# Kernel tuning notes

Measured on AMD Instinct MI355X. Metric: run time of the kernel, lower is better.

Reference implementation:

```python
import jax, jax.numpy as jnp
import numpy as np

NEG_SLOPE = 0.1

def lrelu(x):
    return jnp.where(x >= 0, x, NEG_SLOPE * x)

def conv1d(x, w, b, stride=2):
    # x: [N, C_in, W], w: [C_out, C_in, K], VALID padding, given stride
    y = jax.lax.conv_general_dilated(x, w, (stride,), 'VALID',
                                     dimension_numbers=('NCH', 'OIH', 'NCH'))
    return y + b[None, :, None]

def setup_inputs() -> dict:
    key = jax.random.key(0)
    ks = jax.random.split(key, 16)
    N_NODES = 50000
    N_EDGES = 4950000
    POS_C, CONV_C, CONV_W = 3, 3, 151
    HID, OUT = 256, 1
    W2 = 37  # width after two stride-2 k=3 convs on 151
    IN_G = POS_C + W2  # 40

    def lin_init(k, fan_out, fan_in):
        s = 1.0 / np.sqrt(fan_in)
        k1, k2 = jax.random.split(k)
        return (jax.random.uniform(k1, (fan_out, fan_in), jnp.float32, -s, s),
                jax.random.uniform(k2, (fan_out,), jnp.float32, -s, s))

    pose = jax.random.normal(ks[0], (N_NODES, POS_C), jnp.float32)
    views = jax.random.normal(ks[1], (N_NODES, CONV_C, CONV_W), jnp.float32)
    edge_index = jax.random.randint(ks[2], (2, N_EDGES), 0, N_NODES, jnp.int64)

    # encoder1: Conv1d(3 -> 9, k=3, s=2); encoder2: Conv1d(9 -> 1, k=3, s=2)
    s1 = 1.0 / np.sqrt(CONV_C * 3)
    w_e1 = jax.random.uniform(ks[3], (CONV_C ** 2, CONV_C, 3), jnp.float32, -s1, s1)
    b_e1 = jax.random.uniform(ks[4], (CONV_C ** 2,), jnp.float32, -s1, s1)
    s2 = 1.0 / np.sqrt(CONV_C ** 2 * 3)
    w_e2 = jax.random.uniform(ks[5], (1, CONV_C ** 2, 3), jnp.float32, -s2, s2)
    b_e2 = jax.random.uniform(ks[6], (1,), jnp.float32, -s2, s2)

    # GraphConv: lin_rel (with bias) on aggregated neighbors, lin_root (no bias) on self
    w_rel, b_rel = lin_init(ks[7], HID, IN_G)
    w_root, _ = lin_init(ks[8], HID, IN_G)

    w_l1, b_l1 = lin_init(ks[9], HID, HID)
    w_l2, b_l2 = lin_init(ks[10], HID, HID)
    w_l3, b_l3 = lin_init(ks[11], HID, HID)
    w_pred, b_pred = lin_init(ks[12], OUT, HID)

    return dict(pose=pose, views=views, edge_index=edge_index,
                w_e1=w_e1, b_e1=b_e1, w_e2=w_e2, b_e2=b_e2,
                w_rel=w_rel, b_rel=b_rel, w_root=w_root,
                w_l1=w_l1, b_l1=b_l1, w_l2=w_l2, b_l2=b_l2,
                w_l3=w_l3, b_l3=b_l3, w_pred=w_pred, b_pred=b_pred)

def reference(pose, views, edge_index, w_e1, b_e1, w_e2, b_e2,
              w_rel, b_rel, w_root,
              w_l1, b_l1, w_l2, b_l2, w_l3, b_l3, w_pred, b_pred):
    n_nodes = pose.shape[0]
    # view encoder
    v = lrelu(conv1d(views, w_e1, b_e1))          # [N, 9, 75]
    v = lrelu(conv1d(v, w_e2, b_e2))              # [N, 1, 37]
    x = jnp.concatenate([pose, v[:, 0, :]], axis=1)  # [N, 40]
    # GraphConv (aggr='add'): out = lin_rel(sum_{j->i} x_j) + lin_root(x_i)
    src, dst = edge_index[0], edge_index[1]
    agg = jax.ops.segment_sum(x[src], dst, num_segments=n_nodes)  # [N, 40]
    h = lrelu(agg @ w_rel.T + b_rel + x @ w_root.T)               # [N, 256]
    # MLP stack (dropout is identity in eval mode)
    h = lrelu(h @ w_l1.T + b_l1)
    h = lrelu(h @ w_l2.T + b_l2)
    h = lrelu(h @ w_l3.T + b_l3)
    return h @ w_pred.T + b_pred  # [N, 1]
```

## Files before the change

### kernel.cpp

```cpp
#include <hip/hip_runtime.h>
#include <hip/hip_fp16.h>

#define NEG_SLOPE 0.1f
__device__ __forceinline__ float lrelu(float v) { return fmaxf(v, NEG_SLOPE * v); }

constexpr int CAP = 8704;
constexpr int EPB = 8192;

typedef __attribute__((ext_vector_type(8))) short short8;
typedef __attribute__((ext_vector_type(4))) float f32x4;

__device__ __forceinline__ unsigned short f2bf(float f) {
    union { float f; unsigned u; } v; v.f = f;
    const unsigned r = v.u + 0x7FFF + ((v.u >> 16) & 1);
    return (unsigned short)(r >> 16);
}
__device__ __forceinline__ float bf2f(unsigned short h) {
    union { unsigned u; float f; } v; v.u = ((unsigned)h) << 16;
    return v.f;
}

struct BinSmem {
    int hist[1024], loff[1024], base[1024];
    int wave8[8];
    int pk[EPB];
    unsigned short bkt[EPB];
};
struct EncSmem {
    float w1[81], b1v[9], w2[27], b2v[1];
    float c1[8][9][80];
};

__global__ __launch_bounds__(512) void enc_bin_kernel(
        const int* __restrict__ ei, int* __restrict__ gcur,
        int* __restrict__ pairs, int E, int NB, int NBIN,
        const float* __restrict__ pose, const float* __restrict__ views,
        const float* __restrict__ w1, const float* __restrict__ b1,
        const float* __restrict__ w2, const float* __restrict__ b2,
        const float* __restrict__ w_l1, const float* __restrict__ w_l2,
        const float* __restrict__ w_l3, const float* __restrict__ w_rel,
        const float* __restrict__ w_root,
        unsigned short* __restrict__ Wb1, unsigned short* __restrict__ Wb2,
        unsigned short* __restrict__ Wb3, unsigned short* __restrict__ Wg,
        unsigned short* __restrict__ xHi, unsigned short* __restrict__ xLo,
        __half* __restrict__ xh, int N)
{
    __shared__ __align__(16) char smem_raw[sizeof(BinSmem)];
    const int t = threadIdx.x;

    if (blockIdx.x < (unsigned)NBIN) {
        BinSmem& sm = *reinterpret_cast<BinSmem*>(smem_raw);
        const int lane = t & 63, wid = t >> 6;
        const int e0 = blockIdx.x * EPB + t * 16;
        const int tot = min(E - (int)blockIdx.x * EPB, EPB);

        for (int i = t; i < 1024; i += 512) sm.hist[i] = 0;
        __syncthreads();

        int pk[16], mt[16];
        auto proc = [&](int j, int sv, int dv) {
            const int b = dv >> 6;
            const int r = atomicAdd(&sm.hist[b], 1);
            pk[j] = sv * 80 | ((dv & 63) << 22);
            mt[j] = b | (r << 10);
        };

        if (e0 + 16 <= E) {
            #pragma unroll
            for (int q = 0; q < 4; q++) {
                const int4 sv = *(const int4*)(ei + e0 + 4 * q);
                const int4 dv = *(const int4*)(ei + E + e0 + 4 * q);
                proc(4 * q + 0, sv.x, dv.x);
                proc(4 * q + 1, sv.y, dv.y);
                proc(4 * q + 2, sv.z, dv.z);
                proc(4 * q + 3, sv.w, dv.w);
            }
        } else {
            #pragma unroll
            for (int j = 0; j < 16; j++) {
                mt[j] = -1;
                const int e = e0 + j;
                if (e < E) proc(j, ei[e], ei[E + e]);
            }
        }
        __syncthreads();

        int carry = 0;
        #pragma unroll
        for (int base = 0; base < 1024; base += 512) {
            const int i = base + t;
            const int v = sm.hist[i];
            int sc = v;
            #pragma unroll
            for (int d = 1; d < 64; d <<= 1) {
                const int u = __shfl_up(sc, d);
                if (lane >= d) sc += u;
            }
            if (lane == 63) sm.wave8[wid] = sc;
            __syncthreads();
            if (wid == 0) {
                int wv = (lane < 8) ? sm.wave8[lane] : 0;
                #pragma unroll
                for (int d = 1; d < 8; d <<= 1) {
                    const int u = __shfl_up(wv, d);
                    if (lane >= d) wv += u;
                }
                if (lane < 8) sm.wave8[lane] = wv;
            }
            __syncthreads();
            const int waveoff = (wid > 0) ? sm.wave8[wid - 1] : 0;
            sm.loff[i] = carry + waveoff + sc - v;
            const int chunk_tot = sm.wave8[7];
            __syncthreads();
            carry += chunk_tot;
        }

        for (int i = t; i < NB; i += 512) {
            const int c = sm.hist[i];
            if (c > 0) sm.base[i] = atomicAdd(&gcur[i], c);
        }
        __syncthreads();

        #pragma unroll
        for (int j = 0; j < 16; j++) {
            if (mt[j] >= 0) {
                const int b = mt[j] & 1023;
                const int pos = sm.loff[b] + (mt[j] >> 10);
                sm.pk[pos] = pk[j];
                sm.bkt[pos] = (unsigned short)b;
            }
        }
        __syncthreads();

        for (int i = t; i < tot; i += 512) {
            const int b = sm.bkt[i];
            const int p = sm.base[b] + (i - sm.loff[b]);
            if (p < CAP) pairs[b * CAP + p] = sm.pk[i];
        }
        return;
    }

    EncSmem& sm = *reinterpret_cast<EncSmem*>(smem_raw);
    const int eb = blockIdx.x - NBIN;

    if (eb < 128) {
        const int i = eb * 512 + t;
        Wb1[i] = f2bf(w_l1[i]);
        Wb2[i] = f2bf(w_l2[i]);
        Wb3[i] = f2bf(w_l3[i]);
        if (i < 40960) {
            const int m = i / 160, c = i % 160;
            const int k = c % 80;
            const float v = (k < 40) ? w_rel[m * 40 + k] : w_root[m * 40 + (k - 40)];
            Wg[i] = f2bf(v);
        }
        if (eb == 0 && t < 40) xh[(size_t)N * 40 + t] = __float2half(0.f);
    }

    if (t < 81) sm.w1[t] = w1[t];
    if (t >= 96 && t < 105) sm.b1v[t - 96] = b1[t - 96];
    if (t >= 128 && t < 155) sm.w2[t - 128] = w2[t - 128];
    if (t == 240) sm.b2v[0] = b2[0];
    __syncthreads();

    const int nb = eb * 8;

    #pragma unroll
    for (int pass = 0; pass < 2; pass++) {
        const int task = pass * 512 + t;
        if (task < 600) {
            const int ln = task / 75;
            const int p  = task % 75;
            const int n  = min(nb + ln, N - 1);
            const float* __restrict__ vin = views + (size_t)n * 453 + 2 * p;
            float e[3], o[3], e1[3];
            #pragma unroll
            for (int ic = 0; ic < 3; ic++) {
                const float* ci = vin + ic * 151;
                e[ic] = ci[0]; o[ic] = ci[1]; e1[ic] = ci[2];
            }
            const int didx = (p & 1) * 40 + (p >> 1);
            #pragma unroll
            for (int oc = 0; oc < 9; oc++) {
                float v = sm.b1v[oc];
                #pragma unroll
                for (int ic = 0; ic < 3; ic++)
                    v += sm.w1[oc * 9 + ic * 3 + 0] * e[ic]
                       + sm.w1[oc * 9 + ic * 3 + 1] * o[ic]
                       + sm.w1[oc * 9 + ic * 3 + 2] * e1[ic];
                sm.c1[ln][oc][didx] = lrelu(v);
            }
        }
    }
    __syncthreads();

    if (t < 320) {
        const int ln = t / 40, f = t % 40;
        const int n  = min(nb + ln, N - 1);
        float outv;
        if (f < 3) {
            outv = pose[(size_t)n * 3 + f];
        } else {
            const int ow = f - 3;
            float v = sm.b2v[0];
            #pragma unroll
            for (int ic = 0; ic < 9; ic++)
                v += sm.w2[ic * 3 + 0] * sm.c1[ln][ic][ow]
                   + sm.w2[ic * 3 + 1] * sm.c1[ln][ic][40 + ow]
                   + sm.w2[ic * 3 + 2] * sm.c1[ln][ic][ow + 1];
            outv = lrelu(v);
        }
        const unsigned short hi = f2bf(outv);
        const unsigned short lo = f2bf(outv - bf2f(hi));
        xHi[(size_t)n * 40 + f] = hi;
        xLo[(size_t)n * 40 + f] = lo;
        xh[(size_t)n * 40 + f] = __float2half(outv);
    }
}

__global__ void bucket_sort_kernel(const int* __restrict__ gcur,
                                   const int* __restrict__ pairs,
                                   int* __restrict__ sorted,
                                   int* __restrict__ node_start,
                                   int* __restrict__ node_cnt, int N)
{
    __shared__ int s_cnt[64], s_off[64], s_cur[64];
    const int b = blockIdx.x;
    const int t = threadIdx.x;
    const int cnt = min(gcur[b], CAP);
    const int* __restrict__ pr = pairs + b * CAP;
    int* __restrict__ so = sorted + (size_t)b * CAP;

    if (t < 64) s_cnt[t] = 0;
    __syncthreads();
    for (int i = t; i < cnt; i += 256)
        atomicAdd(&s_cnt[pr[i] >> 22], 1);
    __syncthreads();

    if (t < 64) {
        const int c = s_cnt[t];
        const int p = ((c + 23) / 24) * 24;
        int sc = p;
        #pragma unroll
        for (int d = 1; d < 64; d <<= 1) {
            const int u = __shfl_up(sc, d);
            if (t >= d) sc += u;
        }
        const int excl = sc - p;
        s_off[t] = excl;
        s_cur[t] = excl;
        node_start[b * 64 + t] = b * CAP + excl;
        node_cnt[b * 64 + t] = c;
    }
    __syncthreads();

    if (t < 64) {
        const int e0 = s_off[t] + s_cnt[t];
        const int e1 = s_off[t] + ((s_cnt[t] + 23) / 24) * 24;
        for (int i = e0; i < e1 && i < CAP; i++) so[i] = N * 80;
    }
    for (int i = t; i < cnt; i += 256) {
        const int p = pr[i];
        const int pos = atomicAdd(&s_cur[p >> 22], 1);
        if (pos < CAP) so[pos] = p & 0x3FFFFF;
    }
}

__global__ void gather_sum_kernel(const int* __restrict__ sorted,
                                  const int* __restrict__ node_start,
                                  const int* __restrict__ node_cnt,
                                  const __half* __restrict__ xh,
                                  unsigned short* __restrict__ aggHi,
                                  unsigned short* __restrict__ aggLo, int N)
{
    const int n = blockIdx.x * 4 + (threadIdx.x >> 6);
    const int lane = threadIdx.x & 63;
    if (n >= N) return;

    const int start = node_start[n];
    const int cntp = ((node_cnt[n] + 23) / 24) * 24;
    const int slot = min(lane / 10, 5);
    const int f4 = lane % 10;
    const int* __restrict__ srt = sorted + start + slot;
    const char* __restrict__ xb = (const char*)xh + f4 * 8;

    float ax = 0.f, ay = 0.f, az = 0.f, aw = 0.f;
    for (int e = 0; e < cntp; e += 24) {
        const int o0 = srt[e];
        const int o1 = srt[e + 6];
        const int o2 = srt[e + 12];
        const int o3 = srt[e + 18];
        const uint2 u0 = *(const uint2*)(xb + o0);
        const uint2 u1 = *(const uint2*)(xb + o1);
        const uint2 u2 = *(const uint2*)(xb + o2);
        const uint2 u3 = *(const uint2*)(xb + o3);
        union { unsigned u; __half2 h; } c;
        float2 f;
        c.u = u0.x; f = __half22float2(c.h); ax += f.x; ay += f.y;
        c.u = u0.y; f = __half22float2(c.h); az += f.x; aw += f.y;
        c.u = u1.x; f = __half22float2(c.h); ax += f.x; ay += f.y;
        c.u = u1.y; f = __half22float2(c.h); az += f.x; aw += f.y;
        c.u = u2.x; f = __half22float2(c.h); ax += f.x; ay += f.y;
        c.u = u2.y; f = __half22float2(c.h); az += f.x; aw += f.y;
        c.u = u3.x; f = __half22float2(c.h); ax += f.x; ay += f.y;
        c.u = u3.y; f = __half22float2(c.h); az += f.x; aw += f.y;
    }

    float rx = ax, ry = ay, rz = az, rw = aw;
    #pragma unroll
    for (int s = 10; s <= 50; s += 10) {
        rx += __shfl(ax, f4 + s);
        ry += __shfl(ay, f4 + s);
        rz += __shfl(az, f4 + s);
        rw += __shfl(aw, f4 + s);
    }
    if (lane < 10) {
        ushort4 hi, lo;
        hi.x = f2bf(rx); lo.x = f2bf(rx - bf2f(hi.x));
        hi.y = f2bf(ry); lo.y = f2bf(ry - bf2f(hi.y));
        hi.z = f2bf(rz); lo.z = f2bf(rz - bf2f(hi.z));
        hi.w = f2bf(rw); lo.w = f2bf(rw - bf2f(hi.w));
        *(ushort4*)(aggHi + (size_t)n * 40 + f4 * 4) = hi;
        *(ushort4*)(aggLo + (size_t)n * 40 + f4 * 4) = lo;
    }
}

__device__ __forceinline__ void gemm_tile(const unsigned short* __restrict__ aT,
                                          const unsigned short* __restrict__ W,
                                          int wstride, int K,
                                          int wave, int l16, int q,
                                          f32x4 acc[4][4])
{
    for (int k0 = 0; k0 < K; k0 += 32) {
        short8 af[4], wf[4];
        #pragma unroll
        for (int nt = 0; nt < 4; nt++)
            af[nt] = *(const short8*)(aT + (nt * 16 + l16) * 264 + k0 + q * 8);
        #pragma unroll
        for (int mt = 0; mt < 4; mt++)
            wf[mt] = *(const short8*)(W + (wave * 64 + mt * 16 + l16) * wstride + k0 + q * 8);
        #pragma unroll
        for (int nt = 0; nt < 4; nt++)
            #pragma unroll
            for (int mt = 0; mt < 4; mt++)
                acc[nt][mt] = __builtin_amdgcn_mfma_f32_16x16x32_bf16(af[nt], wf[mt], acc[nt][mt], 0, 0, 0);
    }
}

__device__ __forceinline__ void epi_to_lds(f32x4 acc[4][4], const float* __restrict__ b,
                                           unsigned short* __restrict__ aT,
                                           int wave, int l16, int q)
{
    float bias[4];
    #pragma unroll
    for (int mt = 0; mt < 4; mt++) bias[mt] = b[wave * 64 + mt * 16 + l16];
    #pragma unroll
    for (int nt = 0; nt < 4; nt++)
        #pragma unroll
        for (int r = 0; r < 4; r++)
            #pragma unroll
            for (int mt = 0; mt < 4; mt++) {
                const int row = nt * 16 + q * 4 + r;
                const int col = wave * 64 + mt * 16 + l16;
                aT[row * 264 + col] = f2bf(lrelu(acc[nt][mt][r] + bias[mt]));
            }
}

__global__ void fused_gemm_kernel(const unsigned short* __restrict__ aggHi,
                                  const unsigned short* __restrict__ aggLo,
                                  const unsigned short* __restrict__ xHi,
                                  const unsigned short* __restrict__ xLo,
                                  const unsigned short* __restrict__ Wg,
                                  const float* __restrict__ b_rel,
                                  const unsigned short* __restrict__ Wb1,
                                  const float* __restrict__ b_l1,
                                  const unsigned short* __restrict__ Wb2,
                                  const float* __restrict__ b_l2,
                                  const unsigned short* __restrict__ Wb3,
                                  const float* __restrict__ b_l3,
                                  const float* __restrict__ w_pred,
                                  const float* __restrict__ b_pred,
                                  float* __restrict__ out, int N)
{
    __shared__ __align__(16) unsigned short aT[64 * 264];
    __shared__ float s_part[4][64];
    const int t = threadIdx.x;
    const int n0 = blockIdx.x * 64;
    const int wave = t >> 6, lane = t & 63, q = lane >> 4, l16 = lane & 15;

    for (int u = t; u < 640; u += 256) {
        const int row = u / 10, c = (u % 10) * 4;
        const int srow = min(n0 + row, N - 1);
        const size_t off = (size_t)srow * 40 + c;
        unsigned short* rp = aT + row * 264;
        *(ushort4*)(rp + c)       = *(const ushort4*)(aggHi + off);
        *(ushort4*)(rp + 40 + c)  = *(const ushort4*)(xHi + off);
        *(ushort4*)(rp + 80 + c)  = *(const ushort4*)(aggLo + off);
        *(ushort4*)(rp + 120 + c) = *(const ushort4*)(xLo + off);
    }
    __syncthreads();

    {
        f32x4 acc[4][4] = {};
        gemm_tile(aT, Wg, 160, 160, wave, l16, q, acc);
        __syncthreads();
        epi_to_lds(acc, b_rel, aT, wave, l16, q);
        __syncthreads();
    }
    {
        f32x4 acc[4][4] = {};
        gemm_tile(aT, Wb1, 256, 256, wave, l16, q, acc);
        __syncthreads();
        epi_to_lds(acc, b_l1, aT, wave, l16, q);
        __syncthreads();
    }
    {
        f32x4 acc[4][4] = {};
        gemm_tile(aT, Wb2, 256, 256, wave, l16, q, acc);
        __syncthreads();
        epi_to_lds(acc, b_l2, aT, wave, l16, q);
        __syncthreads();
    }
    {
        f32x4 acc[4][4] = {};
        gemm_tile(aT, Wb3, 256, 256, wave, l16, q, acc);

        float bias[4], wp[4];
        #pragma unroll
        for (int mt = 0; mt < 4; mt++) {
            const int col = wave * 64 + mt * 16 + l16;
            bias[mt] = b_l3[col];
            wp[mt] = w_pred[col];
        }
        #pragma unroll
        for (int nt = 0; nt < 4; nt++)
            #pragma unroll
            for (int r = 0; r < 4; r++) {
                float p = 0.f;
                #pragma unroll
                for (int mt = 0; mt < 4; mt++)
                    p += lrelu(acc[nt][mt][r] + bias[mt]) * wp[mt];
                p += __shfl_xor(p, 1);
                p += __shfl_xor(p, 2);
                p += __shfl_xor(p, 4);
                p += __shfl_xor(p, 8);
                if (l16 == 0) s_part[wave][nt * 16 + q * 4 + r] = p;
            }
        __syncthreads();

        if (t < 64) {
            const int row = n0 + t;
            if (row < N)
                out[row] = s_part[0][t] + s_part[1][t] + s_part[2][t] + s_part[3][t] + b_pred[0];
        }
    }
}

extern "C" void kernel_launch(void* const* d_in, const int* in_sizes, int n_in,
                              void* d_out, int out_size, void* d_ws, size_t ws_size,
                              hipStream_t stream)
{
    const float* pose   = (const float*)d_in[0];
    const float* views  = (const float*)d_in[1];
    const int*   ei     = (const int*)d_in[2];
    const float* w_e1   = (const float*)d_in[3];
    const float* b_e1   = (const float*)d_in[4];
    const float* w_e2   = (const float*)d_in[5];
    const float* b_e2   = (const float*)d_in[6];
    const float* w_rel  = (const float*)d_in[7];
    const float* b_rel  = (const float*)d_in[8];
    const float* w_root = (const float*)d_in[9];
    const float* w_l1   = (const float*)d_in[10];
    const float* b_l1   = (const float*)d_in[11];
    const float* w_l2   = (const float*)d_in[12];
    const float* b_l2   = (const float*)d_in[13];
    const float* w_l3   = (const float*)d_in[14];
    const float* b_l3   = (const float*)d_in[15];
    const float* w_pred = (const float*)d_in[16];
    const float* b_pred = (const float*)d_in[17];
    float* out = (float*)d_out;

    const int N = in_sizes[0] / 3;
    const int E = in_sizes[2] / 2;
    const int NB = (N + 63) >> 6;
    const int NBIN = (E + EPB - 1) / EPB;
    const int ENCB = (N + 7) / 8;
    const int NBLK = (N + 63) / 64;

    unsigned short* xHi = (unsigned short*)d_ws;
    unsigned short* xLo = xHi + (size_t)N * 40;
    unsigned short* aggHi = xLo + (size_t)N * 40;
    unsigned short* aggLo = aggHi + (size_t)N * 40;
    __half* xh = (__half*)(aggLo + (size_t)N * 40);
    int* pairs  = (int*)(xh + (size_t)(N + 1) * 40 + 24);
    int* sorted = pairs + (size_t)NB * CAP;
    int* gcur       = sorted + (size_t)NB * CAP;
    int* node_start = gcur + 1024;
    int* node_cnt   = node_start + NB * 64;
    unsigned short* Wb1 = (unsigned short*)(node_cnt + NB * 64);
    unsigned short* Wb2 = Wb1 + 256 * 256;
    unsigned short* Wb3 = Wb2 + 256 * 256;
    unsigned short* Wg  = Wb3 + 256 * 256;

    hipMemsetAsync(gcur, 0, 1024 * sizeof(int), stream);

    enc_bin_kernel<<<NBIN + ENCB, 512, 0, stream>>>(
        ei, gcur, pairs, E, NB, NBIN,
        pose, views, w_e1, b_e1, w_e2, b_e2,
        w_l1, w_l2, w_l3, w_rel, w_root,
        Wb1, Wb2, Wb3, Wg,
        xHi, xLo, xh, N);

    bucket_sort_kernel<<<NB, 256, 0, stream>>>(gcur, pairs, sorted, node_start, node_cnt, N);
    gather_sum_kernel<<<NB * 16, 256, 0, stream>>>(sorted, node_start, node_cnt, xh, aggHi, aggLo, N);

    fused_gemm_kernel<<<NBLK, 256, 0, stream>>>(
        aggHi, aggLo, xHi, xLo, Wg, b_rel,
        Wb1, b_l1, Wb2, b_l2, Wb3, b_l3,
        w_pred, b_pred, out, N);
}
```

Measured before the change: 370.4 us.

## Fuse bucket sort with gather-sum in shared memory and split encoder from binning

```diff
diff --git a/kernel.cpp b/kernel.cpp
--- a/kernel.cpp
+++ b/kernel.cpp
@@ -20,21 +20,9 @@
     return v.f;
 }
 
-struct BinSmem {
-    int hist[1024], loff[1024], base[1024];
-    int wave8[8];
-    int pk[EPB];
-    unsigned short bkt[EPB];
-};
-struct EncSmem {
-    float w1[81], b1v[9], w2[27], b2v[1];
-    float c1[8][9][80];
-};
-
-__global__ __launch_bounds__(512) void enc_bin_kernel(
-        const int* __restrict__ ei, int* __restrict__ gcur,
-        int* __restrict__ pairs, int E, int NB, int NBIN,
-        const float* __restrict__ pose, const float* __restrict__ views,
+__global__ __launch_bounds__(256) void encoder_kernel(
+        const float* __restrict__ pose,
+        const float* __restrict__ views,
         const float* __restrict__ w1, const float* __restrict__ b1,
         const float* __restrict__ w2, const float* __restrict__ b2,
         const float* __restrict__ w_l1, const float* __restrict__ w_l2,
@@ -42,109 +30,20 @@
         const float* __restrict__ w_root,
         unsigned short* __restrict__ Wb1, unsigned short* __restrict__ Wb2,
         unsigned short* __restrict__ Wb3, unsigned short* __restrict__ Wg,
+        int* __restrict__ gcur,
         unsigned short* __restrict__ xHi, unsigned short* __restrict__ xLo,
         __half* __restrict__ xh, int N)
 {
-    __shared__ __align__(16) char smem_raw[sizeof(BinSmem)];
+    __shared__ float s_w1[81];
+    __shared__ float s_b1[9];
+    __shared__ float s_w2[27];
+    __shared__ float s_b2[1];
+    __shared__ float s_c1[4][9][80];
+
     const int t = threadIdx.x;
 
-    if (blockIdx.x < (unsigned)NBIN) {
-        BinSmem& sm = *reinterpret_cast<BinSmem*>(smem_raw);
-        const int lane = t & 63, wid = t >> 6;
-        const int e0 = blockIdx.x * EPB + t * 16;
-        const int tot = min(E - (int)blockIdx.x * EPB, EPB);
-
-        for (int i = t; i < 1024; i += 512) sm.hist[i] = 0;
-        __syncthreads();
-
-        int pk[16], mt[16];
-        auto proc = [&](int j, int sv, int dv) {
-            const int b = dv >> 6;
-            const int r = atomicAdd(&sm.hist[b], 1);
-            pk[j] = sv * 80 | ((dv & 63) << 22);
-            mt[j] = b | (r << 10);
-        };
-
-        if (e0 + 16 <= E) {
-            #pragma unroll
-            for (int q = 0; q < 4; q++) {
-                const int4 sv = *(const int4*)(ei + e0 + 4 * q);
-                const int4 dv = *(const int4*)(ei + E + e0 + 4 * q);
-                proc(4 * q + 0, sv.x, dv.x);
-                proc(4 * q + 1, sv.y, dv.y);
-                proc(4 * q + 2, sv.z, dv.z);
-                proc(4 * q + 3, sv.w, dv.w);
-            }
-        } else {
-            #pragma unroll
-            for (int j = 0; j < 16; j++) {
-                mt[j] = -1;
-                const int e = e0 + j;
-                if (e < E) proc(j, ei[e], ei[E + e]);
-            }
-        }
-        __syncthreads();
-
-        int carry = 0;
-        #pragma unroll
-        for (int base = 0; base < 1024; base += 512) {
-            const int i = base + t;
-            const int v = sm.hist[i];
-            int sc = v;
-            #pragma unroll
-            for (int d = 1; d < 64; d <<= 1) {
-                const int u = __shfl_up(sc, d);
-                if (lane >= d) sc += u;
-            }
-            if (lane == 63) sm.wave8[wid] = sc;
-            __syncthreads();
-            if (wid == 0) {
-                int wv = (lane < 8) ? sm.wave8[lane] : 0;
-                #pragma unroll
-                for (int d = 1; d < 8; d <<= 1) {
-                    const int u = __shfl_up(wv, d);
-                    if (lane >= d) wv += u;
-                }
-                if (lane < 8) sm.wave8[lane] = wv;
-            }
-            __syncthreads();
-            const int waveoff = (wid > 0) ? sm.wave8[wid - 1] : 0;
-            sm.loff[i] = carry + waveoff + sc - v;
-            const int chunk_tot = sm.wave8[7];
-            __syncthreads();
-            carry += chunk_tot;
-        }
-
-        for (int i = t; i < NB; i += 512) {
-            const int c = sm.hist[i];
-            if (c > 0) sm.base[i] = atomicAdd(&gcur[i], c);
-        }
-        __syncthreads();
-
-        #pragma unroll
-        for (int j = 0; j < 16; j++) {
-            if (mt[j] >= 0) {
-                const int b = mt[j] & 1023;
-                const int pos = sm.loff[b] + (mt[j] >> 10);
-                sm.pk[pos] = pk[j];
-                sm.bkt[pos] = (unsigned short)b;
-            }
-        }
-        __syncthreads();
-
-        for (int i = t; i < tot; i += 512) {
-            const int b = sm.bkt[i];
-            const int p = sm.base[b] + (i - sm.loff[b]);
-            if (p < CAP) pairs[b * CAP + p] = sm.pk[i];
-        }
-        return;
-    }
-
-    EncSmem& sm = *reinterpret_cast<EncSmem*>(smem_raw);
-    const int eb = blockIdx.x - NBIN;
-
-    if (eb < 128) {
-        const int i = eb * 512 + t;
+    if (blockIdx.x < 256) {
+        const int i = blockIdx.x * 256 + t;
         Wb1[i] = f2bf(w_l1[i]);
         Wb2[i] = f2bf(w_l2[i]);
         Wb3[i] = f2bf(w_l3[i]);
@@ -154,21 +53,22 @@
             const float v = (k < 40) ? w_rel[m * 40 + k] : w_root[m * 40 + (k - 40)];
             Wg[i] = f2bf(v);
         }
-        if (eb == 0 && t < 40) xh[(size_t)N * 40 + t] = __float2half(0.f);
-    }
-
-    if (t < 81) sm.w1[t] = w1[t];
-    if (t >= 96 && t < 105) sm.b1v[t - 96] = b1[t - 96];
-    if (t >= 128 && t < 155) sm.w2[t - 128] = w2[t - 128];
-    if (t == 240) sm.b2v[0] = b2[0];
-    __syncthreads();
-
-    const int nb = eb * 8;
+        if (i < 1024) gcur[i] = 0;
+        if (i < 40) xh[(size_t)N * 40 + i] = __float2half(0.f);
+    }
+
+    if (t < 81) s_w1[t] = w1[t];
+    if (t >= 96 && t < 105) s_b1[t - 96] = b1[t - 96];
+    if (t >= 128 && t < 155) s_w2[t - 128] = w2[t - 128];
+    if (t == 240) s_b2[0] = b2[0];
+    __syncthreads();
+
+    const int nb = blockIdx.x * 4;
 
     #pragma unroll
     for (int pass = 0; pass < 2; pass++) {
-        const int task = pass * 512 + t;
-        if (task < 600) {
+        const int task = pass * 256 + t;
+        if (task < 300) {
             const int ln = task / 75;
             const int p  = task % 75;
             const int n  = min(nb + ln, N - 1);
@@ -182,19 +82,19 @@
             const int didx = (p & 1) * 40 + (p >> 1);
             #pragma unroll
             for (int oc = 0; oc < 9; oc++) {
-                float v = sm.b1v[oc];
+                float v = s_b1[oc];
                 #pragma unroll
                 for (int ic = 0; ic < 3; ic++)
-                    v += sm.w1[oc * 9 + ic * 3 + 0] * e[ic]
-                       + sm.w1[oc * 9 + ic * 3 + 1] * o[ic]
-                       + sm.w1[oc * 9 + ic * 3 + 2] * e1[ic];
-                sm.c1[ln][oc][didx] = lrelu(v);
+                    v += s_w1[oc * 9 + ic * 3 + 0] * e[ic]
+                       + s_w1[oc * 9 + ic * 3 + 1] * o[ic]
+                       + s_w1[oc * 9 + ic * 3 + 2] * e1[ic];
+                s_c1[ln][oc][didx] = lrelu(v);
             }
         }
     }
     __syncthreads();
 
-    if (t < 320) {
+    if (t < 160) {
         const int ln = t / 40, f = t % 40;
         const int n  = min(nb + ln, N - 1);
         float outv;
@@ -202,12 +102,12 @@
             outv = pose[(size_t)n * 3 + f];
         } else {
             const int ow = f - 3;
-            float v = sm.b2v[0];
+            float v = s_b2[0];
             #pragma unroll
             for (int ic = 0; ic < 9; ic++)
-                v += sm.w2[ic * 3 + 0] * sm.c1[ln][ic][ow]
-                   + sm.w2[ic * 3 + 1] * sm.c1[ln][ic][40 + ow]
-                   + sm.w2[ic * 3 + 2] * sm.c1[ln][ic][ow + 1];
+                v += s_w2[ic * 3 + 0] * s_c1[ln][ic][ow]
+                   + s_w2[ic * 3 + 1] * s_c1[ln][ic][40 + ow]
+                   + s_w2[ic * 3 + 2] * s_c1[ln][ic][ow + 1];
             outv = lrelu(v);
         }
         const unsigned short hi = f2bf(outv);
@@ -218,22 +118,123 @@
     }
 }
 
-__global__ void bucket_sort_kernel(const int* __restrict__ gcur,
-                                   const int* __restrict__ pairs,
-                                   int* __restrict__ sorted,
-                                   int* __restrict__ node_start,
-                                   int* __restrict__ node_cnt, int N)
-{
+__global__ __launch_bounds__(512) void bin_kernel(
+        const int* __restrict__ ei, int* __restrict__ gcur,
+        int* __restrict__ pairs, int E, int NB)
+{
+    __shared__ int s_hist[1024];
+    __shared__ int s_loff[1024];
+    __shared__ int s_base[1024];
+    __shared__ int s_wave8[8];
+    __shared__ int s_pk[EPB];
+    __shared__ unsigned short s_bkt[EPB];
+    const int t = threadIdx.x;
+    const int lane = t & 63, wid = t >> 6;
+    const int e0 = blockIdx.x * EPB + t * 16;
+    const int tot = min(E - (int)blockIdx.x * EPB, EPB);
+
+    for (int i = t; i < 1024; i += 512) s_hist[i] = 0;
+    __syncthreads();
+
+    int pk[16], mt[16];
+    auto proc = [&](int j, int sv, int dv) {
+        const int b = dv >> 6;
+        const int r = atomicAdd(&s_hist[b], 1);
+        pk[j] = sv * 80 | ((dv & 63) << 22);
+        mt[j] = b | (r << 10);
+    };
+
+    if (e0 + 16 <= E) {
+        #pragma unroll
+        for (int q = 0; q < 4; q++) {
+            const int4 sv = *(const int4*)(ei + e0 + 4 * q);
+            const int4 dv = *(const int4*)(ei + E + e0 + 4 * q);
+            proc(4 * q + 0, sv.x, dv.x);
+            proc(4 * q + 1, sv.y, dv.y);
+            proc(4 * q + 2, sv.z, dv.z);
+            proc(4 * q + 3, sv.w, dv.w);
+        }
+    } else {
+        #pragma unroll
+        for (int j = 0; j < 16; j++) {
+            mt[j] = -1;
+            const int e = e0 + j;
+            if (e < E) proc(j, ei[e], ei[E + e]);
+        }
+    }
+    __syncthreads();
+
+    int carry = 0;
+    #pragma unroll
+    for (int base = 0; base < 1024; base += 512) {
+        const int i = base + t;
+        const int v = s_hist[i];
+        int sc = v;
+        #pragma unroll
+        for (int d = 1; d < 64; d <<= 1) {
+            const int u = __shfl_up(sc, d);
+            if (lane >= d) sc += u;
+        }
+        if (lane == 63) s_wave8[wid] = sc;
+        __syncthreads();
+        if (wid == 0) {
+            int wv = (lane < 8) ? s_wave8[lane] : 0;
+            #pragma unroll
+            for (int d = 1; d < 8; d <<= 1) {
+                const int u = __shfl_up(wv, d);
+                if (lane >= d) wv += u;
+            }
+            if (lane < 8) s_wave8[lane] = wv;
+        }
+        __syncthreads();
+        const int waveoff = (wid > 0) ? s_wave8[wid - 1] : 0;
+        s_loff[i] = carry + waveoff + sc - v;
+        const int chunk_tot = s_wave8[7];
+        __syncthreads();
+        carry += chunk_tot;
+    }
+
+    for (int i = t; i < NB; i += 512) {
+        const int c = s_hist[i];
+        if (c > 0) s_base[i] = atomicAdd(&gcur[i], c);
+    }
+    __syncthreads();
+
+    #pragma unroll
+    for (int j = 0; j < 16; j++) {
+        if (mt[j] >= 0) {
+            const int b = mt[j] & 1023;
+            const int pos = s_loff[b] + (mt[j] >> 10);
+            s_pk[pos] = pk[j];
+            s_bkt[pos] = (unsigned short)b;
+        }
+    }
+    __syncthreads();
+
+    for (int i = t; i < tot; i += 512) {
+        const int b = s_bkt[i];
+        const int p = s_base[b] + (i - s_loff[b]);
+        if (p < CAP) pairs[b * CAP + p] = s_pk[i];
+    }
+}
+
+__global__ __launch_bounds__(512) void sort_gather_kernel(
+        const int* __restrict__ gcur,
+        const int* __restrict__ pairs,
+        const __half* __restrict__ xh,
+        unsigned short* __restrict__ aggHi,
+        unsigned short* __restrict__ aggLo, int N)
+{
+    __shared__ int s_sorted[CAP];
     __shared__ int s_cnt[64], s_off[64], s_cur[64];
     const int b = blockIdx.x;
     const int t = threadIdx.x;
     const int cnt = min(gcur[b], CAP);
-    const int* __restrict__ pr = pairs + b * CAP;
-    int* __restrict__ so = sorted + (size_t)b * CAP;
+    const int* __restrict__ pr = pairs + (size_t)b * CAP;
 
     if (t < 64) s_cnt[t] = 0;
     __syncthreads();
-    for (int i = t; i < cnt; i += 256)
+    for (int i = t; i < cnt; i += 512)
         atomicAdd(&s_cnt[pr[i] >> 22], 1);
     __syncthreads();
 
@@ -249,79 +250,74 @@
         const int excl = sc - p;
         s_off[t] = excl;
         s_cur[t] = excl;
-        node_start[b * 64 + t] = b * CAP + excl;
-        node_cnt[b * 64 + t] = c;
     }
     __syncthreads();
 
     if (t < 64) {
         const int e0 = s_off[t] + s_cnt[t];
         const int e1 = s_off[t] + ((s_cnt[t] + 23) / 24) * 24;
-        for (int i = e0; i < e1 && i < CAP; i++) so[i] = N * 80;
-    }
-    for (int i = t; i < cnt; i += 256) {
+        for (int i = e0; i < e1 && i < CAP; i++) s_sorted[i] = N * 80;
+    }
+    for (int i = t; i < cnt; i += 512) {
         const int p = pr[i];
         const int pos = atomicAdd(&s_cur[p >> 22], 1);
-        if (pos < CAP) so[pos] = p & 0x3FFFFF;
-    }
-}
-
-__global__ void gather_sum_kernel(const int* __restrict__ sorted,
-                                  const int* __restrict__ node_start,
-                                  const int* __restrict__ node_cnt,
-                                  const __half* __restrict__ xh,
-                                  unsigned short* __restrict__ aggHi,
-                                  unsigned short* __restrict__ aggLo, int N)
-{
-    const int n = blockIdx.x * 4 + (threadIdx.x >> 6);
-    const int lane = threadIdx.x & 63;
-    if (n >= N) return;
-
-    const int start = node_start[n];
-    const int cntp = ((node_cnt[n] + 23) / 24) * 24;
+        if (pos < CAP) s_sorted[pos] = p & 0x3FFFFF;
+    }
+    __syncthreads();
+
+    const int wave = t >> 6, lane = t & 63;
     const int slot = min(lane / 10, 5);
     const int f4 = lane % 10;
-    const int* __restrict__ srt = sorted + start + slot;
     const char* __restrict__ xb = (const char*)xh + f4 * 8;
 
-    float ax = 0.f, ay = 0.f, az = 0.f, aw = 0.f;
-    for (int e = 0; e < cntp; e += 24) {
-        const int o0 = srt[e];
-        const int o1 = srt[e + 6];
-        const int o2 = srt[e + 12];
-        const int o3 = srt[e + 18];
-        const uint2 u0 = *(const uint2*)(xb + o0);
-        const uint2 u1 = *(const uint2*)(xb + o1);
-        const uint2 u2 = *(const uint2*)(xb + o2);
-        const uint2 u3 = *(const uint2*)(xb + o3);
-        union { unsigned u; __half2 h; } c;
-        float2 f;
-        c.u = u0.x; f = __half22float2(c.h); ax += f.x; ay += f.y;
-        c.u = u0.y; f = __half22float2(c.h); az += f.x; aw += f.y;
-        c.u = u1.x; f = __half22float2(c.h); ax += f.x; ay += f.y;
-        c.u = u1.y; f = __half22float2(c.h); az += f.x; aw += f.y;
-        c.u = u2.x; f = __half22float2(c.h); ax += f.x; ay += f.y;
-        c.u = u2.y; f = __half22float2(c.h); az += f.x; aw += f.y;
-        c.u = u3.x; f = __half22float2(c.h); ax += f.x; ay += f.y;
-        c.u = u3.y; f = __half22float2(c.h); az += f.x; aw += f.y;
-    }
-
-    float rx = ax, ry = ay, rz = az, rw = aw;
-    #pragma unroll
-    for (int s = 10; s <= 50; s += 10) {
-        rx += __shfl(ax, f4 + s);
-        ry += __shfl(ay, f4 + s);
-        rz += __shfl(az, f4 + s);
-        rw += __shfl(aw, f4 + s);
-    }
-    if (lane < 10) {
-        ushort4 hi, lo;
-        hi.x = f2bf(rx); lo.x = f2bf(rx - bf2f(hi.x));
-        hi.y = f2bf(ry); lo.y = f2bf(ry - bf2f(hi.y));
-        hi.z = f2bf(rz); lo.z = f2bf(rz - bf2f(hi.z));
-        hi.w = f2bf(rw); lo.w = f2bf(rw - bf2f(hi.w));
-        *(ushort4*)(aggHi + (size_t)n * 40 + f4 * 4) = hi;
-        *(ushort4*)(aggLo + (size_t)n * 40 + f4 * 4) = lo;
+    #pragma unroll 1
+    for (int i = 0; i < 8; i++) {
+        const int ln = wave * 8 + i;
+        const int n = b * 64 + ln;
+        if (n >= N) break;
+        const int c = s_cnt[ln];
+        const int cntp = ((c + 23) / 24) * 24;
+        const int* __restrict__ srt = s_sorted + s_off[ln] + slot;
+
+        float ax = 0.f, ay = 0.f, az = 0.f, aw = 0.f;
+        for (int e = 0; e < cntp; e += 24) {
+            const int o0 = srt[e];
+            const int o1 = srt[e + 6];
+            const int o2 = srt[e + 12];
+            const int o3 = srt[e + 18];
+            const uint2 u0 = *(const uint2*)(xb + o0);
+            const uint2 u1 = *(const uint2*)(xb + o1);
+            const uint2 u2 = *(const uint2*)(xb + o2);
+            const uint2 u3 = *(const uint2*)(xb + o3);
+            union { unsigned u; __half2 h; } cv;
+            float2 f;
+            cv.u = u0.x; f = __half22float2(cv.h); ax += f.x; ay += f.y;
+            cv.u = u0.y; f = __half22float2(cv.h); az += f.x; aw += f.y;
+            cv.u = u1.x; f = __half22float2(cv.h); ax += f.x; ay += f.y;
+            cv.u = u1.y; f = __half22float2(cv.h); az += f.x; aw += f.y;
+            cv.u = u2.x; f = __half22float2(cv.h); ax += f.x; ay += f.y;
+            cv.u = u2.y; f = __half22float2(cv.h); az += f.x; aw += f.y;
+            cv.u = u3.x; f = __half22float2(cv.h); ax += f.x; ay += f.y;
+            cv.u = u3.y; f = __half22float2(cv.h); az += f.x; aw += f.y;
+        }
+
+        float rx = ax, ry = ay, rz = az, rw = aw;
+        #pragma unroll
+        for (int s = 10; s <= 50; s += 10) {
+            rx += __shfl(ax, f4 + s);
+            ry += __shfl(ay, f4 + s);
+            rz += __shfl(az, f4 + s);
+            rw += __shfl(aw, f4 + s);
+        }
+        if (lane < 10) {
+            ushort4 hi, lo;
+            hi.x = f2bf(rx); lo.x = f2bf(rx - bf2f(hi.x));
+            hi.y = f2bf(ry); lo.y = f2bf(ry - bf2f(hi.y));
+            hi.z = f2bf(rz); lo.z = f2bf(rz - bf2f(hi.z));
+            hi.w = f2bf(rw); lo.w = f2bf(rw - bf2f(hi.w));
+            *(ushort4*)(aggHi + (size_t)n * 40 + f4 * 4) = hi;
+            *(ushort4*)(aggLo + (size_t)n * 40 + f4 * 4) = lo;
+        }
     }
 }
 
@@ -483,8 +479,6 @@
     const int N = in_sizes[0] / 3;
     const int E = in_sizes[2] / 2;
     const int NB = (N + 63) >> 6;
-    const int NBIN = (E + EPB - 1) / EPB;
-    const int ENCB = (N + 7) / 8;
     const int NBLK = (N + 63) / 64;
 
     unsigned short* xHi = (unsigned short*)d_ws;
@@ -492,27 +486,21 @@
     unsigned short* aggHi = xLo + (size_t)N * 40;
     unsigned short* aggLo = aggHi + (size_t)N * 40;
     __half* xh = (__half*)(aggLo + (size_t)N * 40);
-    int* pairs  = (int*)(xh + (size_t)(N + 1) * 40 + 24);
-    int* sorted = pairs + (size_t)NB * CAP;
-    int* gcur       = sorted + (size_t)NB * CAP;
-    int* node_start = gcur + 1024;
-    int* node_cnt   = node_start + NB * 64;
-    unsigned short* Wb1 = (unsigned short*)(node_cnt + NB * 64);
+    int* pairs = (int*)(xh + (size_t)(N + 1) * 40 + 24);
+    int* gcur  = pairs + (size_t)NB * CAP;
+    unsigned short* Wb1 = (unsigned short*)(gcur + 1024);
     unsigned short* Wb2 = Wb1 + 256 * 256;
     unsigned short* Wb3 = Wb2 + 256 * 256;
     unsigned short* Wg  = Wb3 + 256 * 256;
 
-    hipMemsetAsync(gcur, 0, 1024 * sizeof(int), stream);
-
-    enc_bin_kernel<<<NBIN + ENCB, 512, 0, stream>>>(
-        ei, gcur, pairs, E, NB, NBIN,
+    encoder_kernel<<<(N + 3) / 4, 256, 0, stream>>>(
         pose, views, w_e1, b_e1, w_e2, b_e2,
         w_l1, w_l2, w_l3, w_rel, w_root,
-        Wb1, Wb2, Wb3, Wg,
-        xHi, xLo, xh, N);
-
-    bucket_sort_kernel<<<NB, 256, 0, stream>>>(gcur, pairs, sorted, node_start, node_cnt, N);
-    gather_sum_kernel<<<NB * 16, 256, 0, stream>>>(sorted, node_start, node_cnt, xh, aggHi, aggLo, N);
+        Wb1, Wb2, Wb3, Wg, gcur, xHi, xLo, xh, N);
+
+    bin_kernel<<<(E + EPB - 1) / EPB, 512, 0, stream>>>(ei, gcur, pairs, E, NB);
+
+    sort_gather_kernel<<<NB, 512, 0, stream>>>(gcur, pairs, xh, aggHi, aggLo, N);
 
     fused_gemm_kernel<<<NBLK, 256, 0, stream>>>(
         aggHi, aggLo, xHi, xLo, Wg, b_rel,
```

Result: faster. 342.9 us (-7.4%).
